# Optimization experiments

Measured on AMD Instinct MI355X. Metric: run time of the kernel, lower is better.

The kernel has to match this reference:

```python
import jax, jax.numpy as jnp
import numpy as np

B, K, D = 1024, 262144, 64

def setup_inputs() -> dict:
    key = jax.random.key(0)
    k1, k2 = jax.random.split(key)
    query_vec = jax.random.normal(k1, (B, D), dtype=jnp.float32)
    memory = jax.random.normal(k2, (K, D), dtype=jnp.float32)
    return {"query_vec": query_vec, "memory": memory, "topk": 5}

def reference(query_vec, memory, topk):
    # sim: [B, K] similarity against the full memory bank
    sim = jnp.einsum('bd,kd->bk', query_vec, memory)
    # indices of top-k most similar bank rows: [B, topk]
    _, topk_idx = jax.lax.top_k(sim, topk)
    # gather rows: [B, topk, D]
    return memory[topk_idx]
```

## Files before the change

### kernel.cpp

```cpp
#include <hip/hip_runtime.h>
#include <stdint.h>

typedef unsigned long long u64;
typedef __attribute__((ext_vector_type(8))) short short8;
typedef __attribute__((ext_vector_type(4))) float f32x4;

#define KROWS  262144
#define DDIM   64
#define NQ     1024
#define NC     256
#define CHUNK  (KROWS / NC)
#define SUB    128
#define NSUB   (CHUNK / SUB)
#define KC_PER 4
#define BIAS   128.0f
#define SIMMASK 0xFFFFFC00u

__device__ __forceinline__ uint32_t ord32(float f) {
    uint32_t u = __float_as_uint(f);
    return (u & 0x80000000u) ? ~u : (u | 0x80000000u);
}
__device__ __forceinline__ uint32_t maxu(uint32_t a, uint32_t b) { return a > b ? a : b; }
__device__ __forceinline__ uint32_t minu(uint32_t a, uint32_t b) { return a < b ? a : b; }
__device__ __forceinline__ void fold2(uint32_t& t0, uint32_t& t1, uint32_t k) {
    t1 = maxu(t1, minu(t0, k));
    t0 = maxu(t0, k);
}
__device__ __forceinline__ void fold4(uint32_t (&t)[4], uint32_t k) {
    uint32_t n1 = maxu(t[1], minu(t[0], k));
    uint32_t n2 = maxu(t[2], minu(t[1], k));
    uint32_t n3 = maxu(t[3], minu(t[2], k));
    t[0] = maxu(t[0], k);
    t[1] = n1; t[2] = n2; t[3] = n3;
}
__device__ __forceinline__ uint32_t bf16rne(float f) {
    uint32_t u = __float_as_uint(f);
    return (u + 0x7fffu + ((u >> 16) & 1u)) >> 16;
}
__device__ __forceinline__ uint32_t pack2(float a, float b) {
    return bf16rne(a) | (bf16rne(b) << 16);
}
__device__ __forceinline__ void gload_lds16(const void* g, void* l) {
    __builtin_amdgcn_global_load_lds(
        (const __attribute__((address_space(1))) uint32_t*)g,
        (__attribute__((address_space(3))) uint32_t*)l, 16, 0, 0);
}

__global__ __launch_bounds__(256) void conv(const float* __restrict__ Mf,
                                            uint16_t* __restrict__ Mb) {
    const int stride = gridDim.x * 256;
    const float4* src = (const float4*)Mf;
    uint4* dst = (uint4*)Mb;
    for (int e = blockIdx.x * 256 + threadIdx.x; e < (KROWS * DDIM / 8); e += stride) {
        const float4 a = src[2 * e], b = src[2 * e + 1];
        uint4 o;
        o.x = pack2(a.x, a.y); o.y = pack2(a.z, a.w);
        o.z = pack2(b.x, b.y); o.w = pack2(b.z, b.w);
        dst[e] = o;
    }
}

__global__ __launch_bounds__(512, 4) void p1(const float* __restrict__ Qg,
                                             const uint16_t* __restrict__ Mb,
                                             uint32_t* __restrict__ wsK) {
    __shared__ __align__(16) uint16_t stage[2 * 8192];
    const int t = threadIdx.x;
    const int lane = t & 63;
    const int w = t >> 6;
    const int quad = lane >> 4;
    const int m = lane & 15;
    const int qcol = blockIdx.x;
    const int chunk = blockIdx.y;
    const int qBase = qcol * 256 + w * 32;
    const int rowChunk = chunk * CHUNK;

    short8 afr[2][2];
    #pragma unroll
    for (int qt = 0; qt < 2; ++qt)
        #pragma unroll
        for (int kh = 0; kh < 2; ++kh) {
            const float* qp = Qg + (size_t)(qBase + qt * 16 + m) * DDIM + quad * 8 + kh * 32;
            const float4 f0 = ((const float4*)qp)[0];
            const float4 f1 = ((const float4*)qp)[1];
            short8 a;
            a[0] = (short)bf16rne(f0.x); a[1] = (short)bf16rne(f0.y);
            a[2] = (short)bf16rne(f0.z); a[3] = (short)bf16rne(f0.w);
            a[4] = (short)bf16rne(f1.x); a[5] = (short)bf16rne(f1.y);
            a[6] = (short)bf16rne(f1.z); a[7] = (short)bf16rne(f1.w);
            afr[qt][kh] = a;
        }
    const f32x4 bias = {BIAS, BIAS, BIAS, BIAS};

    uint32_t tA[8], tB[8];
    #pragma unroll
    for (int li = 0; li < 8; ++li) { tA[li] = 0u; tB[li] = 0u; }

    auto stage_sub = [&](int sb, int buf) {
        const uint16_t* src = Mb + (size_t)(rowChunk + sb * SUB) * DDIM;
        #pragma unroll
        for (int i = 0; i < 2; ++i) {
            const int slotBase = w * 128 + i * 64;
            const int slot = slotBase + lane;
            const int row = slot >> 3, c = slot & 7;
            const int g = row * 8 + (c ^ (row & 7));
            gload_lds16(src + (size_t)g * 8, stage + buf * 8192 + slotBase * 8);
        }
    };

    stage_sub(0, 0);
    #pragma unroll 2
    for (int sb = 0; sb < NSUB; ++sb) {
        __syncthreads();
        if (sb + 1 < NSUB) stage_sub(sb + 1, (sb + 1) & 1);
        const uint16_t* bufp = stage + (sb & 1) * 8192;
        const uint32_t pb = (uint32_t)m + (uint32_t)sb * 128u;
        #pragma unroll
        for (int rt = 0; rt < 8; ++rt) {
            const int r = rt * 16 + m;
            const short8 b0 = *(const short8*)(bufp + r * 64 + ((quad       ^ (m & 7)) * 8));
            const short8 b1 = *(const short8*)(bufp + r * 64 + (((quad + 4) ^ (m & 7)) * 8));
            f32x4 c0, c1;
            c0 = __builtin_amdgcn_mfma_f32_16x16x32_bf16(afr[0][0], b0, bias, 0, 0, 0);
            c0 = __builtin_amdgcn_mfma_f32_16x16x32_bf16(afr[0][1], b1, c0,   0, 0, 0);
            c1 = __builtin_amdgcn_mfma_f32_16x16x32_bf16(afr[1][0], b0, bias, 0, 0, 0);
            c1 = __builtin_amdgcn_mfma_f32_16x16x32_bf16(afr[1][1], b1, c1,   0, 0, 0);
            const uint32_t posm = pb + (uint32_t)(rt * 16);
            #pragma unroll
            for (int reg = 0; reg < 4; ++reg) {
                fold2(tA[reg],     tB[reg],     (__float_as_uint(c0[reg]) & SIMMASK) | posm);
                fold2(tA[4 + reg], tB[4 + reg], (__float_as_uint(c1[reg]) & SIMMASK) | posm);
            }
        }
    }

    #pragma unroll
    for (int g = 0; g < 2; ++g) {
        uint32_t fl[4][4];
        #pragma unroll
        for (int r4 = 0; r4 < 4; ++r4) {
            fl[r4][0] = tA[g * 4 + r4]; fl[r4][1] = tB[g * 4 + r4];
            fl[r4][2] = 0u;             fl[r4][3] = 0u;
        }
        #pragma unroll
        for (int d = 1; d <= 8; d <<= 1) {
            const int nv = (d == 1) ? 2 : 4;
            #pragma unroll
            for (int r4 = 0; r4 < 4; ++r4) {
                uint32_t rm[4];
                #pragma unroll
                for (int s = 0; s < 4; ++s)
                    if (s < nv) rm[s] = __shfl_xor(fl[r4][s], d, 64);
                #pragma unroll
                for (int s = 0; s < 4; ++s)
                    if (s < nv) fold4(fl[r4], rm[s]);
            }
        }
        if (m == 0) {
            #pragma unroll
            for (int r4 = 0; r4 < 4; ++r4) {
                const int q = qBase + g * 16 + quad * 4 + r4;
                uint4 v4; v4.x = fl[r4][0]; v4.y = fl[r4][1];
                v4.z = fl[r4][2]; v4.w = fl[r4][3];
                *(uint4*)(wsK + ((size_t)chunk * NQ + (size_t)q) * KC_PER) = v4;
            }
        }
    }
}

__global__ __launch_bounds__(64) void p2(const float* __restrict__ Qg,
                                         const float* __restrict__ Mf,
                                         const uint32_t* __restrict__ wsK,
                                         float* __restrict__ out) {
    const int Q = blockIdx.x;
    const int lane = threadIdx.x;
    u64 mk[16];
    #pragma unroll
    for (int i = 0; i < 4; ++i) {
        const int c = i * 64 + lane;
        const uint4 k4 = *(const uint4*)(wsK + ((size_t)c * NQ + (size_t)Q) * KC_PER);
        const uint32_t cb = (uint32_t)c * (uint32_t)CHUNK;
        mk[i * 4 + 0] = ((u64)k4.x << 32) | (u64)(cb + (k4.x & 1023u));
        mk[i * 4 + 1] = ((u64)k4.y << 32) | (u64)(cb + (k4.y & 1023u));
        mk[i * 4 + 2] = ((u64)k4.z << 32) | (u64)(cb + (k4.z & 1023u));
        mk[i * 4 + 3] = ((u64)k4.w << 32) | (u64)(cb + (k4.w & 1023u));
    }
    uint32_t idxs[16];
    #pragma unroll
    for (int it = 0; it < 16; ++it) {
        u64 wk = mk[0];
        #pragma unroll
        for (int i2 = 1; i2 < 16; ++i2) wk = mk[i2] > wk ? mk[i2] : wk;
        #pragma unroll
        for (int off = 32; off >= 1; off >>= 1) {
            const u64 o = __shfl_xor(wk, off, 64);
            wk = o > wk ? o : wk;
        }
        #pragma unroll
        for (int i2 = 0; i2 < 16; ++i2) if (mk[i2] == wk) mk[i2] = 0;
        idxs[it] = (uint32_t)wk & (KROWS - 1u);
    }
    const float qv = Qg[(size_t)Q * DDIM + lane];
    float v[16];
    #pragma unroll
    for (int j = 0; j < 16; ++j) v[j] = Mf[(size_t)idxs[j] * DDIM + lane];
    u64 rk[16];
    #pragma unroll
    for (int j = 0; j < 16; ++j) {
        float p = qv * v[j];
        #pragma unroll
        for (int off = 32; off >= 1; off >>= 1) p += __shfl_xor(p, off, 64);
        rk[j] = ((u64)ord32(p) << 32) | (u64)(~idxs[j]);
    }
    #pragma unroll
    for (int it = 0; it < 5; ++it) {
        u64 best = rk[0];
        #pragma unroll
        for (int j = 1; j < 16; ++j) best = rk[j] > best ? rk[j] : best;
        float o = 0.f;
        #pragma unroll
        for (int j = 0; j < 16; ++j) o = (rk[j] == best) ? v[j] : o;
        out[((size_t)Q * 5 + it) * DDIM + lane] = o;
        #pragma unroll
        for (int j = 0; j < 16; ++j) rk[j] = (rk[j] == best) ? 0ull : rk[j];
    }
}

extern "C" void kernel_launch(void* const* d_in, const int* in_sizes, int n_in,
                              void* d_out, int out_size, void* d_ws, size_t ws_size,
                              hipStream_t stream) {
    const float* Qg = (const float*)d_in[0];
    const float* Mf = (const float*)d_in[1];
    float* out = (float*)d_out;
    uint32_t* wsK = (uint32_t*)d_ws;
    uint16_t* Mb = (uint16_t*)((char*)d_ws + (4u << 20));

    conv<<<2048, 256, 0, stream>>>(Mf, Mb);
    p1<<<dim3(4, NC), 512, 0, stream>>>(Qg, Mb, wsK);
    p2<<<NQ, 64, 0, stream>>>(Qg, Mf, wsK, out);
}
```

Before: 188.3 us.

## Fuse bf16 conversion of memory bank into p1 staging loads

Removes the separate conv kernel that turned the fp32 memory bank into bf16 in workspace. p1 now reads fp32 rows directly into registers, converts them to bf16 and writes them to the swizzled LDS buffer, prefetching the next subtile across the MFMA loop. This saves a full write and re-read of the 32MB bf16 copy and one launch. In exchange, the 4 query-column blocks each re-read the fp32 data (twice the bytes of bf16), and staging goes through registers instead of async global_load_lds. Separately, p2 now packs four queries per 256-thread block.

```diff
diff --git a/kernel.cpp b/kernel.cpp
--- a/kernel.cpp
+++ b/kernel.cpp
@@ -40,28 +40,9 @@
 __device__ __forceinline__ uint32_t pack2(float a, float b) {
     return bf16rne(a) | (bf16rne(b) << 16);
 }
-__device__ __forceinline__ void gload_lds16(const void* g, void* l) {
-    __builtin_amdgcn_global_load_lds(
-        (const __attribute__((address_space(1))) uint32_t*)g,
-        (__attribute__((address_space(3))) uint32_t*)l, 16, 0, 0);
-}
-
-__global__ __launch_bounds__(256) void conv(const float* __restrict__ Mf,
-                                            uint16_t* __restrict__ Mb) {
-    const int stride = gridDim.x * 256;
-    const float4* src = (const float4*)Mf;
-    uint4* dst = (uint4*)Mb;
-    for (int e = blockIdx.x * 256 + threadIdx.x; e < (KROWS * DDIM / 8); e += stride) {
-        const float4 a = src[2 * e], b = src[2 * e + 1];
-        uint4 o;
-        o.x = pack2(a.x, a.y); o.y = pack2(a.z, a.w);
-        o.z = pack2(b.x, b.y); o.w = pack2(b.z, b.w);
-        dst[e] = o;
-    }
-}
 
 __global__ __launch_bounds__(512, 4) void p1(const float* __restrict__ Qg,
-                                             const uint16_t* __restrict__ Mb,
+                                             const float* __restrict__ Mf,
                                              uint32_t* __restrict__ wsK) {
     __shared__ __align__(16) uint16_t stage[2 * 8192];
     const int t = threadIdx.x;
@@ -95,35 +76,45 @@
     #pragma unroll
     for (int li = 0; li < 8; ++li) { tA[li] = 0u; tB[li] = 0u; }
 
-    auto stage_sub = [&](int sb, int buf) {
-        const uint16_t* src = Mb + (size_t)(rowChunk + sb * SUB) * DDIM;
-        #pragma unroll
-        for (int i = 0; i < 2; ++i) {
-            const int slotBase = w * 128 + i * 64;
-            const int slot = slotBase + lane;
-            const int row = slot >> 3, c = slot & 7;
-            const int g = row * 8 + (c ^ (row & 7));
-            gload_lds16(src + (size_t)g * 8, stage + buf * 8192 + slotBase * 8);
-        }
+    const int sr0 = t >> 3,          sc0 = (t & 7) ^ (sr0 & 7);
+    const int sr1 = (t + 512) >> 3,  sc1 = (t & 7) ^ (sr1 & 7);
+    auto ld = [&](int sb, float4& a0, float4& a1, float4& b0, float4& b1) {
+        const float* base = Mf + (size_t)(rowChunk + sb * SUB) * DDIM;
+        const float4* p0 = (const float4*)(base + sr0 * DDIM + sc0 * 8);
+        const float4* p1p = (const float4*)(base + sr1 * DDIM + sc1 * 8);
+        a0 = p0[0]; a1 = p0[1];
+        b0 = p1p[0]; b1 = p1p[1];
     };
-
-    stage_sub(0, 0);
+    auto st = [&](int buf, float4 a0, float4 a1, float4 b0, float4 b1) {
+        uint16_t* bp = stage + buf * 8192;
+        uint4 w0, w1;
+        w0.x = pack2(a0.x, a0.y); w0.y = pack2(a0.z, a0.w);
+        w0.z = pack2(a1.x, a1.y); w0.w = pack2(a1.z, a1.w);
+        w1.x = pack2(b0.x, b0.y); w1.y = pack2(b0.z, b0.w);
+        w1.z = pack2(b1.x, b1.y); w1.w = pack2(b1.z, b1.w);
+        *(uint4*)(bp + (size_t)t * 8) = w0;
+        *(uint4*)(bp + (size_t)(t + 512) * 8) = w1;
+    };
+
+    float4 a0, a1, b0, b1;
+    ld(0, a0, a1, b0, b1);
+    st(0, a0, a1, b0, b1);
     #pragma unroll 2
     for (int sb = 0; sb < NSUB; ++sb) {
+        if (sb + 1 < NSUB) ld(sb + 1, a0, a1, b0, b1);
         __syncthreads();
-        if (sb + 1 < NSUB) stage_sub(sb + 1, (sb + 1) & 1);
         const uint16_t* bufp = stage + (sb & 1) * 8192;
         const uint32_t pb = (uint32_t)m + (uint32_t)sb * 128u;
         #pragma unroll
         for (int rt = 0; rt < 8; ++rt) {
             const int r = rt * 16 + m;
-            const short8 b0 = *(const short8*)(bufp + r * 64 + ((quad       ^ (m & 7)) * 8));
-            const short8 b1 = *(const short8*)(bufp + r * 64 + (((quad + 4) ^ (m & 7)) * 8));
+            const short8 v0 = *(const short8*)(bufp + r * 64 + ((quad       ^ (m & 7)) * 8));
+            const short8 v1 = *(const short8*)(bufp + r * 64 + (((quad + 4) ^ (m & 7)) * 8));
             f32x4 c0, c1;
-            c0 = __builtin_amdgcn_mfma_f32_16x16x32_bf16(afr[0][0], b0, bias, 0, 0, 0);
-            c0 = __builtin_amdgcn_mfma_f32_16x16x32_bf16(afr[0][1], b1, c0,   0, 0, 0);
-            c1 = __builtin_amdgcn_mfma_f32_16x16x32_bf16(afr[1][0], b0, bias, 0, 0, 0);
-            c1 = __builtin_amdgcn_mfma_f32_16x16x32_bf16(afr[1][1], b1, c1,   0, 0, 0);
+            c0 = __builtin_amdgcn_mfma_f32_16x16x32_bf16(afr[0][0], v0, bias, 0, 0, 0);
+            c0 = __builtin_amdgcn_mfma_f32_16x16x32_bf16(afr[0][1], v1, c0,   0, 0, 0);
+            c1 = __builtin_amdgcn_mfma_f32_16x16x32_bf16(afr[1][0], v0, bias, 0, 0, 0);
+            c1 = __builtin_amdgcn_mfma_f32_16x16x32_bf16(afr[1][1], v1, c1,   0, 0, 0);
             const uint32_t posm = pb + (uint32_t)(rt * 16);
             #pragma unroll
             for (int reg = 0; reg < 4; ++reg) {
@@ -131,6 +122,7 @@
                 fold2(tA[4 + reg], tB[4 + reg], (__float_as_uint(c1[reg]) & SIMMASK) | posm);
             }
         }
+        if (sb + 1 < NSUB) st((sb + 1) & 1, a0, a1, b0, b1);
     }
 
     #pragma unroll
@@ -167,12 +159,12 @@
     }
 }
 
-__global__ __launch_bounds__(64) void p2(const float* __restrict__ Qg,
-                                         const float* __restrict__ Mf,
-                                         const uint32_t* __restrict__ wsK,
-                                         float* __restrict__ out) {
-    const int Q = blockIdx.x;
-    const int lane = threadIdx.x;
+__global__ __launch_bounds__(256) void p2(const float* __restrict__ Qg,
+                                          const float* __restrict__ Mf,
+                                          const uint32_t* __restrict__ wsK,
+                                          float* __restrict__ out) {
+    const int Q = blockIdx.x * 4 + (threadIdx.x >> 6);
+    const int lane = threadIdx.x & 63;
     u64 mk[16];
     #pragma unroll
     for (int i = 0; i < 4; ++i) {
@@ -232,9 +224,7 @@
     const float* Mf = (const float*)d_in[1];
     float* out = (float*)d_out;
     uint32_t* wsK = (uint32_t*)d_ws;
-    uint16_t* Mb = (uint16_t*)((char*)d_ws + (4u << 20));
-
-    conv<<<2048, 256, 0, stream>>>(Mf, Mb);
-    p1<<<dim3(4, NC), 512, 0, stream>>>(Qg, Mb, wsK);
-    p2<<<NQ, 64, 0, stream>>>(Qg, Mf, wsK, out);
-}
+
+    p1<<<dim3(4, NC), 512, 0, stream>>>(Qg, Mf, wsK);
+    p2<<<NQ / 4, 256, 0, stream>>>(Qg, Mf, wsK, out);
+}
```

Result: slower. 362.1 us (+92.3%).
